# Kernel optimization log

Measured on AMD Instinct MI355X. Metric: run time of the kernel, lower is better.

Reference implementation:

```python
import jax, jax.numpy as jnp
import numpy as np

EPS = 1e-5  # RMSNorm epsilon


def rmsnorm(x, w):
    return x * jax.lax.rsqrt(jnp.mean(x * x, axis=-1, keepdims=True) + EPS) * w


def mamba_forward(u, in_proj_w, conv_w, conv_b, x_proj_w, dt_proj_w, dt_proj_b,
                  A_log, D_param, mamba_out_w):
    # u: (b, L, dm) -- canonical Mamba block (expand=2, d_state=16, d_conv=4)
    b, L, dm = u.shape
    di, ds = A_log.shape
    dtr = dt_proj_w.shape[1]
    xz = jnp.einsum('bld,ed->ble', u, in_proj_w)          # (b,L,2*di)
    x_, z = jnp.split(xz, 2, axis=-1)                     # each (b,L,di)
    # causal depthwise conv over the sequence axis
    dconv = conv_w.shape[-1]
    xc = jnp.transpose(x_, (0, 2, 1))                     # (b,di,L)
    xc = jnp.pad(xc, ((0, 0), (0, 0), (dconv - 1, 0)))
    xc = jax.lax.conv_general_dilated(xc, conv_w, window_strides=(1,), padding='VALID',
                                      dimension_numbers=('NCH', 'OIH', 'NCH'),
                                      feature_group_count=di)
    xc = xc + conv_b[None, :, None]
    x_ = jax.nn.silu(jnp.transpose(xc, (0, 2, 1)))        # (b,L,di)
    # input-dependent dt, B, C
    x_dbl = jnp.einsum('bld,ed->ble', x_, x_proj_w)       # (b,L,dtr+2*ds)
    dt, B, C = jnp.split(x_dbl, [dtr, dtr + ds], axis=-1)
    delta = jax.nn.softplus(jnp.einsum('blr,dr->bld', dt, dt_proj_w) + dt_proj_b)  # (b,L,di)
    A = -jnp.exp(A_log)                                   # (di,ds)

    def step(h, inp):
        d_t, B_t, C_t, x_t = inp                          # (b,di),(b,ds),(b,ds),(b,di)
        dA = jnp.exp(d_t[:, :, None] * A)                 # (b,di,ds)
        h = dA * h + (d_t * x_t)[:, :, None] * B_t[:, None, :]
        y = jnp.einsum('bds,bs->bd', h, C_t)
        return h, y

    xs = (jnp.moveaxis(delta, 1, 0), jnp.moveaxis(B, 1, 0),
          jnp.moveaxis(C, 1, 0), jnp.moveaxis(x_, 1, 0))
    h0 = jnp.zeros((b, di, ds), dtype=u.dtype)
    _, ys = jax.lax.scan(step, h0, xs)                    # ys: (L,b,di)
    y = jnp.moveaxis(ys, 0, 1) + x_ * D_param             # (b,L,di)
    y = y * jax.nn.silu(z)
    return jnp.einsum('bld,od->blo', y, mamba_out_w)      # (b,L,dm)


def conv1x1(W, bvec, t):
    # t: (b, cin, L) -> (b, cout, L)
    return jnp.einsum('oi,bit->bot', W, t) + bvec[None, :, None]


def reference(x, w_norm1, w_norm2, W_ip, b_ip, W_fp, b_fp, W_wp, b_wp, W_op, b_op,
              in_proj_w, conv_w, conv_b, x_proj_w, dt_proj_w, dt_proj_b,
              A_log, D_param, mamba_out_w):
    # x: (b, L, D) -- module's (b, c, l) with l == input_dim = D, c == seq = L
    residual = x
    xn = rmsnorm(x, w_norm1)                 # RMSNorm over last (input_dim) axis
    xt = jnp.transpose(xn, (0, 2, 1))        # 'b c l -> b l c' : (b, D, L)
    ssm = conv1x1(W_ip, b_ip, xt)            # (b, 2D, L)
    ssm = conv1x1(W_fp, b_fp, ssm)           # (b, 2D, L)
    u = jnp.transpose(ssm, (0, 2, 1))        # (b, L, 2D): seq=L, d_model=2D
    m = mamba_forward(u, in_proj_w, conv_w, conv_b, x_proj_w, dt_proj_w, dt_proj_b,
                      A_log, D_param, mamba_out_w)
    m = rmsnorm(m, w_norm2) + u              # PostNormMamba residual
    ssm = jnp.transpose(m, (0, 2, 1))        # (b, 2D, L)
    w = conv1x1(W_wp, b_wp, xt)              # (b, 2D, L)
    w = w * jax.nn.sigmoid(w)                # swish
    out = conv1x1(W_op, b_op, w * ssm)       # (b, D, L)
    return jnp.transpose(out, (0, 2, 1)) + residual


def setup_inputs():
    key = jax.random.key(0)
    ks = jax.random.split(key, 16)
    D, L, b = 64, 4096, 4
    dm, di, ds, dconv = 2 * D, 4 * D, 16, 4
    dtr = (dm + 15) // 16  # dt_rank = ceil(d_model/16) = 8

    def n(k, shape, fan_in):
        return jax.random.normal(k, shape, jnp.float32) * (1.0 / np.sqrt(fan_in))

    return {
        'x': jax.random.normal(ks[0], (b, L, D), jnp.float32),
        'w_norm1': jnp.ones((D,), jnp.float32),
        'w_norm2': jnp.ones((dm,), jnp.float32),
        'W_ip': n(ks[1], (2 * D, D), D), 'b_ip': jnp.zeros((2 * D,), jnp.float32),
        'W_fp': n(ks[2], (2 * D, 2 * D), 2 * D), 'b_fp': jnp.zeros((2 * D,), jnp.float32),
        'W_wp': n(ks[3], (2 * D, D), D), 'b_wp': jnp.zeros((2 * D,), jnp.float32),
        'W_op': n(ks[4], (D, 2 * D), 2 * D), 'b_op': jnp.zeros((D,), jnp.float32),
        'in_proj_w': n(ks[5], (2 * di, dm), dm),
        'conv_w': n(ks[6], (di, 1, dconv), dconv),
        'conv_b': jnp.zeros((di,), jnp.float32),
        'x_proj_w': n(ks[7], (dtr + 2 * ds, di), di),
        'dt_proj_w': n(ks[8], (di, dtr), dtr),
        'dt_proj_b': jnp.full((di,), float(np.log(np.expm1(0.01))), jnp.float32),
        'A_log': jnp.log(jnp.broadcast_to(jnp.arange(1, ds + 1, dtype=jnp.float32), (di, ds))),
        'D_param': jnp.ones((di,), jnp.float32),
        'mamba_out_w': n(ks[9], (dm, di), di),
    }
```

## Files before the change

### kernel.cpp

```cpp
#include <hip/hip_runtime.h>
#include <hip/hip_bf16.h>

typedef __hip_bfloat16 bf16;
typedef __attribute__((ext_vector_type(8))) short bf16x8;
typedef __attribute__((ext_vector_type(4))) float f32x4;
#define DEV __device__ __forceinline__

constexpr int SEQ  = 4096;
constexpr int NB   = 4;
constexpr int NTOK = NB * SEQ;
constexpr float EPS = 1e-5f;
constexpr int NCH = 32;
constexpr int NCHUNK = SEQ / NCH;
constexpr float LOG2E = 1.44269504f;

constexpr int OFF_WDT  = 0;
constexpr int OFF_WB   = 2048;
constexpr int WB_IP = 0;
constexpr int WB_WP = 8192;
constexpr int WB_FP = 16384;
constexpr int WB_PR = 32768;
constexpr int WB_MO = 98304;
constexpr int WB_OP = 131072;
constexpr int WB_XP = 139264;
constexpr int WB_TOT = 151552;
constexpr int OFF_XDBL = OFF_WB + WB_TOT / 2;
constexpr int OFF_R1   = OFF_XDBL + NTOK * 40;
constexpr int OFF_WSW  = OFF_R1   + 1048576;
constexpr int OFF_U    = OFF_WSW  + 1048576;
constexpr int OFF_R2   = OFF_U    + 1048576;
constexpr int OFF_SILUZ= OFF_R2   + 2097152;
constexpr int OFF_XC   = OFF_SILUZ+ 2097152;
constexpr int OFF_G    = OFF_XC   + 2097152;
constexpr int OFF_FLAG = OFF_G    + 2097152;
constexpr int OFF_SUMM = OFF_FLAG + 16;
constexpr int OFF_HIN  = OFF_SUMM + 64 * NCHUNK * 256 * 2;
constexpr int OFF_PLOC = OFF_HIN  + 64 * NCHUNK * 256;
constexpr int OFF_CUMD = OFF_PLOC + NTOK * 256;

DEV float b2f(bf16 x) { return __bfloat162float(x); }
DEV bf16 f2b(float x) { return __float2bfloat16(x); }
DEV short shof(bf16 h) { short s; __builtin_memcpy(&s, &h, 2); return s; }
DEV float ldin(const void* p, int i, int f) {
  return f ? ((const float*)p)[i] : b2f(((const bf16*)p)[i]);
}
DEV unsigned pack2(float a, float b) {
  bf16 ha = f2b(a), hb = f2b(b);
  unsigned short ua, ub;
  __builtin_memcpy(&ua, &ha, 2); __builtin_memcpy(&ub, &hb, 2);
  return (unsigned)ua | ((unsigned)ub << 16);
}
DEV float lo16f(unsigned u) { return __int_as_float((int)(u << 16)); }
DEV float hi16f(unsigned u) { return __int_as_float((int)(u & 0xffff0000u)); }
template<int CTRL>
DEV float dpp_add(float v) {
  int r = __builtin_amdgcn_update_dpp(0, __float_as_int(v), CTRL, 0xF, 0xF, false);
  return v + __int_as_float(r);
}
DEV float exp2f_fast(float a) { return __builtin_amdgcn_exp2f(a); }
DEV float softplus(float a) {
  return (a > 20.f) ? a : __logf(1.f + exp2f_fast(a * LOG2E));
}
DEV float silu(float a) { return a / (1.f + __expf(-a)); }

DEV void cpw(int e, int base, int count, const void* __restrict__ src,
             bf16* __restrict__ wb, int f) {
  int r = e - base;
  if (r >= 0 && r < count) wb[base + r] = f2b(ldin(src, r, f));
}
__global__ __launch_bounds__(256) void prep_k(
    const void* __restrict__ w_ip, const void* __restrict__ w_wp, const void* __restrict__ w_fp,
    const void* __restrict__ w_pr, const void* __restrict__ w_mo, const void* __restrict__ w_op,
    const void* __restrict__ w_x,  const void* __restrict__ w_dt,
    const void* __restrict__ x, float* __restrict__ wsf, int* __restrict__ flagp)
{
  __shared__ int cnt;
  if (threadIdx.x == 0) cnt = 0;
  __syncthreads();
  {
    float v = b2f(((const bf16*)x)[threadIdx.x]);
    int ok = (v == v) && fabsf(v) > 1e-4f && fabsf(v) < 100.f;
    atomicAdd(&cnt, ok);
  }
  __syncthreads();
  int f = (cnt > 204) ? 0 : 1;
  if (blockIdx.x == 0 && threadIdx.x == 0) *flagp = f;

  int e = blockIdx.x * 256 + threadIdx.x;
  bf16* wb = (bf16*)(wsf + OFF_WB);
  cpw(e, WB_IP, 8192,  w_ip, wb, f);
  cpw(e, WB_WP, 8192,  w_wp, wb, f);
  cpw(e, WB_FP, 16384, w_fp, wb, f);
  cpw(e, WB_PR, 65536, w_pr, wb, f);
  cpw(e, WB_MO, 32768, w_mo, wb, f);
  cpw(e, WB_OP, 8192,  w_op, wb, f);
  {
    int r = e - WB_XP;
    if (r >= 0 && r < 12288) wb[WB_XP + r] = (r < 10240) ? f2b(ldin(w_x, r, f)) : f2b(0.f);
  }
  if (e < 2048) {
    int r = e >> 8, d = e & 255;
    wsf[OFF_WDT + e] = ldin(w_dt, d * 8 + r, f);
  }
}

__global__ __launch_bounds__(512) void fm_k(
    const void* __restrict__ x, const void* __restrict__ w1, const float* __restrict__ wsf,
    const void* __restrict__ b_ip, const void* __restrict__ b_wp, const void* __restrict__ b_fp,
    bf16* __restrict__ wsw, bf16* __restrict__ u, bf16* __restrict__ xpre,
    bf16* __restrict__ siluz, const int* __restrict__ flagp)
{
  __shared__ __align__(16) char smem[33280];
  short* xn   = (short*)smem;
  short* t1   = (short*)(smem + 4608);
  short* ul   = (short*)(smem + 13312);
  short* wswl = (short*)(smem + 22016);
  short* xzl  = (short*)smem;

  const int f = *flagp;
  const int tid = threadIdx.x;
  const int tok0 = blockIdx.x * 32;
  {
    const int token = tid >> 4, r = tid & 15;
    float v[4]; float ss = 0.f;
    #pragma unroll
    for (int k = 0; k < 4; ++k) {
      v[k] = ldin(x, (tok0 + token) * 64 + r * 4 + k, f);
      ss += v[k] * v[k];
    }
    ss += __shfl_xor(ss, 1, 16); ss += __shfl_xor(ss, 2, 16);
    ss += __shfl_xor(ss, 4, 16); ss += __shfl_xor(ss, 8, 16);
    float sc = rsqrtf(ss * (1.f / 64.f) + EPS);
    unsigned* dst = (unsigned*)xn + token * 36 + r * 2;
    #pragma unroll
    for (int k = 0; k < 2; ++k) {
      int i = r * 4 + k * 2;
      dst[k] = pack2(v[k*2] * sc * ldin(w1, i, f), v[k*2+1] * sc * ldin(w1, i + 1, f));
    }
  }
  __syncthreads();
  const int lane = tid & 63, m = lane & 15, q = lane >> 4;
  const int w = tid >> 6;
  {
    const int wt = w >> 2, ng = w & 3;
    const bf16* W = (const bf16*)(wsf + OFF_WB) + (wt ? WB_WP : WB_IP);
    const void* bia = wt ? b_wp : b_ip;
    bf16x8 a[2][2];
    #pragma unroll
    for (int mt = 0; mt < 2; ++mt)
      #pragma unroll
      for (int kk = 0; kk < 2; ++kk)
        a[mt][kk] = *(const bf16x8*)&xn[(mt * 16 + m) * 72 + kk * 32 + q * 8];
    #pragma unroll
    for (int nti = 0; nti < 2; ++nti) {
      int nt = ng * 2 + nti;
      int n = nt * 16 + m;
      f32x4 acc[2] = {{0,0,0,0},{0,0,0,0}};
      #pragma unroll
      for (int kk = 0; kk < 2; ++kk) {
        bf16x8 b = *(const bf16x8*)(W + (nt * 16 + m) * 64 + kk * 32 + q * 8);
        #pragma unroll
        for (int mt = 0; mt < 2; ++mt)
          acc[mt] = __builtin_amdgcn_mfma_f32_16x16x32_bf16(a[mt][kk], b, acc[mt], 0, 0, 0);
      }
      float bv = ldin(bia, n, f);
      #pragma unroll
      for (int mt = 0; mt < 2; ++mt)
        #pragma unroll
        for (int r = 0; r < 4; ++r) {
          float v = acc[mt][r] + bv;
          int row = mt * 16 + q * 4 + r;
          if (wt) wswl[row * 128 + n] = shof(f2b(silu(v)));
          else    t1[row * 136 + n] = shof(f2b(v));
        }
    }
  }
  __syncthreads();
  {
    int row = tid >> 4, c8 = (tid & 15) * 8;
    uint4 v = *(const uint4*)&wswl[row * 128 + c8];
    *(uint4*)(wsw + (tok0 + row) * 128 + c8) = v;
  }
  {
    const bf16* WF = (const bf16*)(wsf + OFF_WB) + WB_FP;
    bf16x8 a[2][4];
    #pragma unroll
    for (int mt = 0; mt < 2; ++mt)
      #pragma unroll
      for (int kk = 0; kk < 4; ++kk)
        a[mt][kk] = *(const bf16x8*)&t1[(mt * 16 + m) * 136 + kk * 32 + q * 8];
    {
      int nt = w;
      int n = nt * 16 + m;
      f32x4 acc[2] = {{0,0,0,0},{0,0,0,0}};
      #pragma unroll
      for (int kk = 0; kk < 4; ++kk) {
        bf16x8 b = *(const bf16x8*)(WF + (nt * 16 + m) * 128 + kk * 32 + q * 8);
        #pragma unroll
        for (int mt = 0; mt < 2; ++mt)
          acc[mt] = __builtin_amdgcn_mfma_f32_16x16x32_bf16(a[mt][kk], b, acc[mt], 0, 0, 0);
      }
      float bv = ldin(b_fp, n, f);
      #pragma unroll
      for (int mt = 0; mt < 2; ++mt)
        #pragma unroll
        for (int r = 0; r < 4; ++r)
          ul[(mt * 16 + q * 4 + r) * 136 + n] = shof(f2b(acc[mt][r] + bv));
    }
  }
  __syncthreads();
  {
    int row = tid >> 4, c8 = (tid & 15) * 8;
    uint4 v = *(const uint4*)&ul[row * 136 + c8];
    *(uint4*)(u + (tok0 + row) * 128 + c8) = v;
  }
  {
    const bf16* WP = (const bf16*)(wsf + OFF_WB) + WB_PR;
    bf16x8 a[2][4];
    #pragma unroll
    for (int mt = 0; mt < 2; ++mt)
      #pragma unroll
      for (int kk = 0; kk < 4; ++kk)
        a[mt][kk] = *(const bf16x8*)&ul[(mt * 16 + m) * 136 + kk * 32 + q * 8];
    __syncthreads();
    #pragma unroll
    for (int nti = 0; nti < 4; ++nti) {
      int nt = w * 4 + nti;
      int n = nt * 16 + m;
      f32x4 acc[2] = {{0,0,0,0},{0,0,0,0}};
      #pragma unroll
      for (int kk = 0; kk < 4; ++kk) {
        bf16x8 b = *(const bf16x8*)(WP + (nt * 16 + m) * 128 + kk * 32 + q * 8);
        #pragma unroll
        for (int mt = 0; mt < 2; ++mt)
          acc[mt] = __builtin_amdgcn_mfma_f32_16x16x32_bf16(a[mt][kk], b, acc[mt], 0, 0, 0);
      }
      #pragma unroll
      for (int mt = 0; mt < 2; ++mt)
        #pragma unroll
        for (int r = 0; r < 4; ++r) {
          int row = mt * 16 + q * 4 + r;
          float v = acc[mt][r];
          xzl[row * 520 + n] = shof(f2b(n < 256 ? v : silu(v)));
        }
    }
  }
  __syncthreads();
  {
    #pragma unroll
    for (int k = 0; k < 4; ++k) {
      int chunk = tid + k * 512;
      int row = chunk >> 6, seg = chunk & 63;
      uint4 v = *(const uint4*)&xzl[row * 520 + seg * 8];
      int n0 = seg * 8;
      if (n0 < 256) *(uint4*)(xpre + (tok0 + row) * 256 + n0) = v;
      else          *(uint4*)(siluz + (tok0 + row) * 256 + (n0 - 256)) = v;
    }
  }
}

__global__ __launch_bounds__(256) void conv_k(
    const bf16* __restrict__ xpre, const void* __restrict__ cw, const void* __restrict__ cb,
    const float* __restrict__ wsf, bf16* __restrict__ xc, float* __restrict__ xdbl,
    const int* __restrict__ flagp)
{
  __shared__ short xh[35 * 256];
  __shared__ short cs[32 * 264];
  const int f = *flagp;
  const int tid = threadIdx.x;
  const int tok0 = blockIdx.x * 32;
  const bool seqstart = (tok0 & (SEQ - 1)) == 0;
  for (int c = tid; c < 1120; c += 256) {
    int e0 = c * 8;
    int tt = e0 >> 8, i = e0 & 255;
    int gtok = tok0 + tt - 3;
    uint4* dst = (uint4*)(xh + e0);
    if (gtok >= 0 && !(seqstart && tt < 3)) *dst = *(const uint4*)(xpre + gtok * 256 + i);
    else                                    *dst = make_uint4(0, 0, 0, 0);
  }
  __syncthreads();
  {
    const int ch0 = (tid & 63) * 4;
    const int t0 = (tid >> 6) * 8;
    float w4[4][4], cb4[4];
    #pragma unroll
    for (int c = 0; c < 4; ++c) {
      cb4[c] = ldin(cb, ch0 + c, f);
      #pragma unroll
      for (int k = 0; k < 4; ++k) w4[c][k] = ldin(cw, (ch0 + c) * 4 + k, f);
    }
    float win[11][4];
    #pragma unroll
    for (int r = 0; r < 11; ++r) {
      uint2 v = *(const uint2*)&xh[(t0 + r) * 256 + ch0];
      win[r][0] = lo16f(v.x); win[r][1] = hi16f(v.x);
      win[r][2] = lo16f(v.y); win[r][3] = hi16f(v.y);
    }
    #pragma unroll
    for (int t = 0; t < 8; ++t) {
      unsigned pk[2];
      #pragma unroll
      for (int cp = 0; cp < 2; ++cp) {
        float o[2];
        #pragma unroll
        for (int ci = 0; ci < 2; ++ci) {
          int c = cp * 2 + ci;
          float acc = cb4[c];
          #pragma unroll
          for (int k = 0; k < 4; ++k) acc = fmaf(win[t + k][c], w4[c][k], acc);
          o[ci] = silu(acc);
        }
        pk[cp] = pack2(o[0], o[1]);
      }
      uint2 pv = make_uint2(pk[0], pk[1]);
      *(uint2*)&cs[(t0 + t) * 264 + ch0] = pv;
      *(uint2*)(xc + (tok0 + t0 + t) * 256 + ch0) = pv;
    }
  }
  __syncthreads();
  const int w = tid >> 6;
  if (w < 2) {
    const bf16* Wx = (const bf16*)(wsf + OFF_WB) + WB_XP;
    const int lane = tid & 63, m = lane & 15, quad = lane >> 4;
    f32x4 acc[3] = {{0,0,0,0},{0,0,0,0},{0,0,0,0}};
    #pragma unroll
    for (int k0 = 0; k0 < 256; k0 += 32) {
      bf16x8 af = *(const bf16x8*)&cs[(w * 16 + m) * 264 + k0 + quad * 8];
      #pragma unroll
      for (int nt = 0; nt < 3; ++nt) {
        bf16x8 bfr = *(const bf16x8*)(Wx + (nt * 16 + m) * 256 + k0 + quad * 8);
        acc[nt] = __builtin_amdgcn_mfma_f32_16x16x32_bf16(af, bfr, acc[nt], 0, 0, 0);
      }
    }
    #pragma unroll
    for (int nt = 0; nt < 3; ++nt) {
      int n = nt * 16 + m;
      if (n < 40) {
        #pragma unroll
        for (int r = 0; r < 4; ++r)
          xdbl[(tok0 + w * 16 + quad * 4 + r) * 40 + n] = acc[nt][r];
      }
    }
  }
}

__global__ __launch_bounds__(256) void scanF_k(
    const float* __restrict__ xdbl, const bf16* __restrict__ xc,
    const void* __restrict__ A_log, const void* __restrict__ dt_b,
    const float* __restrict__ WDT, float* __restrict__ summ,
    float* __restrict__ ploc, float* __restrict__ cumd, const int* __restrict__ flagp)
{
  const int f = *flagp;
  const int tid = threadIdx.x;
  const int bb = blockIdx.x >> 2, dgsup = blockIdx.x & 3, c = blockIdx.y;
  const int dgsub = tid >> 6, lane = tid & 63, dl = lane >> 2, squad = lane & 3;
  const int dg = dgsup * 4 + dgsub;
  const int bxOld = bb * 16 + dg;
  const int d_comp = dg * 16 + dl;
  const int bd = tid & 63;
  const int d_stg = dgsup * 64 + bd;
  const int bdc = dgsub * 16 + dl;
  const int tok_base = bb * SEQ + c * NCH;

  __shared__ float dt_l[NCH * 8];
  __shared__ float dx_l[16 * 64 * 2];
  __shared__ float Bp[16 * 16];
  __shared__ float Cp[16 * 16];
  __shared__ float pg_l[16 * 64];
  __shared__ float cd_l[16 * 64];

  float Aval2[4];
  #pragma unroll
  for (int j = 0; j < 4; ++j)
    Aval2[j] = -__expf(ldin(A_log, d_comp * 16 + squad * 4 + j, f)) * LOG2E;
  const float dtb_stg = ldin(dt_b, d_stg, f);
  float wdt[8];
  #pragma unroll
  for (int r = 0; r < 8; ++r) wdt[r] = WDT[r * 256 + d_stg];

  float h[4] = {0.f, 0.f, 0.f, 0.f};
  float sdlt = 0.f;

  if (tid < 64)
    *(float4*)(dt_l + tid * 4) = *(const float4*)(xdbl + (tok_base + (tid >> 1)) * 40 + (tid & 1) * 4);

  #pragma unroll 1
  for (int half = 0; half < 2; ++half) {
    const int tb = half * 16;
    __syncthreads();
    {
      int tl = tid >> 4, s = tid & 15;
      int tok = tok_base + tb + tl;
      Bp[tid] = xdbl[tok * 40 + 8 + s];
      Cp[tid] = xdbl[tok * 40 + 24 + s];
    }
    #pragma unroll
    for (int k = 0; k < 4; ++k) {
      int tl = (tid >> 6) + k * 4;
      int tok = tok_base + tb + tl;
      const float* dtr = dt_l + (tb + tl) * 8;
      float a = dtb_stg;
      #pragma unroll
      for (int r = 0; r < 8; ++r) a = fmaf(dtr[r], wdt[r], a);
      float dlt = softplus(a);
      float xcv = b2f(xc[tok * 256 + d_stg]);
      *(float2*)(dx_l + (tl * 64 + bd) * 2) = make_float2(dlt, dlt * xcv);
    }
    __syncthreads();

    #pragma unroll 8
    for (int tl = 0; tl < 16; ++tl) {
      float2 dx = *(const float2*)(dx_l + (tl * 64 + bdc) * 2);
      float4 B4 = *(const float4*)(Bp + tl * 16 + squad * 4);
      float Bv[4] = {B4.x, B4.y, B4.z, B4.w};
      #pragma unroll
      for (int j = 0; j < 4; ++j) {
        float dA = exp2f_fast(dx.x * Aval2[j]);
        h[j] = fmaf(dA, h[j], dx.y * Bv[j]);
      }
      sdlt += dx.x;
      float4 C4 = *(const float4*)(Cp + tl * 16 + squad * 4);
      float p = h[0] * C4.x;
      p = fmaf(h[1], C4.y, p);
      p = fmaf(h[2], C4.z, p);
      p = fmaf(h[3], C4.w, p);
      p = dpp_add<0xB1>(p);
      p = dpp_add<0x4E>(p);
      if (squad == 0) { pg_l[tl * 64 + bdc] = p; cd_l[tl * 64 + bdc] = sdlt; }
    }
    __syncthreads();
    #pragma unroll
    for (int k = 0; k < 4; ++k) {
      int tl = (tid >> 6) + k * 4;
      int tok = tok_base + tb + tl;
      ploc[tok * 256 + d_stg] = pg_l[tl * 64 + bd];
      cumd[tok * 256 + d_stg] = cd_l[tl * 64 + bd];
    }
  }

  float* dst = summ + ((bxOld * NCHUNK + c) * 256 + dl * 16 + squad * 4) * 2;
  *(float4*)(dst)     = make_float4(exp2f_fast(Aval2[0] * sdlt), h[0],
                                    exp2f_fast(Aval2[1] * sdlt), h[1]);
  *(float4*)(dst + 4) = make_float4(exp2f_fast(Aval2[2] * sdlt), h[2],
                                    exp2f_fast(Aval2[3] * sdlt), h[3]);
}

__global__ __launch_bounds__(256) void scanB_k(const float* __restrict__ summ, float* __restrict__ hinit) {
  int bx = blockIdx.x, qq = threadIdx.x;
  float h = 0.f;
  for (int c0 = 0; c0 < NCHUNK; c0 += 16) {
    float2 sv[16];
    #pragma unroll
    for (int k = 0; k < 16; ++k)
      sv[k] = *(const float2*)(summ + ((bx * NCHUNK + c0 + k) * 256 + qq) * 2);
    #pragma unroll
    for (int k = 0; k < 16; ++k) {
      hinit[(bx * NCHUNK + c0 + k) * 256 + qq] = h;
      h = fmaf(sv[k].x, h, sv[k].y);
    }
  }
}

__global__ __launch_bounds__(256) void scanC_k(
    const float* __restrict__ xdbl, const bf16* __restrict__ xc, const bf16* __restrict__ siluz,
    const void* __restrict__ A_log, const void* __restrict__ D_par,
    const float* __restrict__ hinit, const float* __restrict__ ploc,
    const float* __restrict__ cumd, bf16* __restrict__ g, const int* __restrict__ flagp)
{
  const int f = *flagp;
  const int tid = threadIdx.x;
  const int bb = blockIdx.x >> 2, dgsup = blockIdx.x & 3, c = blockIdx.y;
  const int dgsub = tid >> 6, lane = tid & 63, dl = lane >> 2, squad = lane & 3;
  const int dg = dgsup * 4 + dgsub;
  const int bxOld = bb * 16 + dg;
  const int d_comp = dg * 16 + dl;
  const int bd = tid & 63;
  const int d_stg = dgsup * 64 + bd;
  const int bdc = dgsub * 16 + dl;
  const int tok_base = bb * SEQ + c * NCH;

  __shared__ float Cp[NCH * 16];
  __shared__ float cd_l[NCH * 64];
  __shared__ float g_l[NCH * 64];

  float Aval2[4];
  #pragma unroll
  for (int j = 0; j < 4; ++j)
    Aval2[j] = -__expf(ldin(A_log, d_comp * 16 + squad * 4 + j, f)) * LOG2E;
  const float Dp_stg = ldin(D_par, d_stg, f);

  float4 hv = *(const float4*)(hinit + (bxOld * NCHUNK + c) * 256 + dl * 16 + squad * 4);

  #pragma unroll
  for (int k = 0; k < 2; ++k) {
    int e = tid + k * 256;
    int tl = e >> 4, s = e & 15;
    Cp[e] = xdbl[(tok_base + tl) * 40 + 24 + s];
  }
  #pragma unroll
  for (int k = 0; k < 8; ++k) {
    int tl = (tid >> 6) + k * 4;
    cd_l[tl * 64 + bd] = cumd[(tok_base + tl) * 256 + d_stg];
  }
  __syncthreads();

  #pragma unroll 8
  for (int tl = 0; tl < NCH; ++tl) {
    float cum = cd_l[tl * 64 + bdc];
    float4 C4 = *(const float4*)(Cp + tl * 16 + squad * 4);
    float p =      C4.x * exp2f_fast(cum * Aval2[0]) * hv.x;
    p = fmaf(C4.y * exp2f_fast(cum * Aval2[1]), hv.y, p);
    p = fmaf(C4.z * exp2f_fast(cum * Aval2[2]), hv.z, p);
    p = fmaf(C4.w * exp2f_fast(cum * Aval2[3]), hv.w, p);
    p = dpp_add<0xB1>(p);
    p = dpp_add<0x4E>(p);
    if (squad == 0) g_l[tl * 64 + bdc] = p;
  }
  __syncthreads();

  #pragma unroll
  for (int k = 0; k < 8; ++k) {
    int tl = (tid >> 6) + k * 4;
    int tok = tok_base + tl;
    float pf = ploc[tok * 256 + d_stg] + g_l[tl * 64 + bd];
    float xcv = b2f(xc[tok * 256 + d_stg]);
    g[tok * 256 + d_stg] = f2b((pf + xcv * Dp_stg) * b2f(siluz[tok * 256 + d_stg]));
  }
}

__global__ __launch_bounds__(512) void back_k(
    const bf16* __restrict__ g, const float* __restrict__ wsf, const void* __restrict__ w2,
    const bf16* __restrict__ u, const bf16* __restrict__ wsw, const void* __restrict__ b_op,
    const void* __restrict__ x, void* __restrict__ out, const int* __restrict__ flagp)
{
  __shared__ __align__(16) short ms[32 * 136];
  const int f = *flagp;
  const int tid = threadIdx.x;
  const int tok0 = blockIdx.x * 32;
  const int lane = tid & 63, m = lane & 15, q = lane >> 4;
  const int w = tid >> 6;
  const bf16* WM = (const bf16*)(wsf + OFF_WB) + WB_MO;
  const bf16* WO = (const bf16*)(wsf + OFF_WB) + WB_OP;
  {
    f32x4 acc[2] = {{0,0,0,0},{0,0,0,0}};
    #pragma unroll
    for (int kk = 0; kk < 8; ++kk) {
      bf16x8 a0 = *(const bf16x8*)(g + (tok0 + m) * 256 + kk * 32 + q * 8);
      bf16x8 a1 = *(const bf16x8*)(g + (tok0 + 16 + m) * 256 + kk * 32 + q * 8);
      int nt = w;
      bf16x8 b = *(const bf16x8*)(WM + (nt * 16 + m) * 256 + kk * 32 + q * 8);
      acc[0] = __builtin_amdgcn_mfma_f32_16x16x32_bf16(a0, b, acc[0], 0, 0, 0);
      acc[1] = __builtin_amdgcn_mfma_f32_16x16x32_bf16(a1, b, acc[1], 0, 0, 0);
    }
    {
      int n = w * 16 + m;
      #pragma unroll
      for (int mt = 0; mt < 2; ++mt)
        #pragma unroll
        for (int r = 0; r < 4; ++r)
          ms[(mt * 16 + q * 4 + r) * 136 + n] = shof(f2b(acc[mt][r]));
    }
  }
  __syncthreads();
  {
    const int token = tid >> 4, r = tid & 15;
    float mv[8]; float ss = 0.f;
    #pragma unroll
    for (int k = 0; k < 8; ++k) {
      mv[k] = b2f(((const bf16*)ms)[token * 136 + r * 8 + k]);
      ss += mv[k] * mv[k];
    }
    ss += __shfl_xor(ss, 1, 16); ss += __shfl_xor(ss, 2, 16);
    ss += __shfl_xor(ss, 4, 16); ss += __shfl_xor(ss, 8, 16);
    float sc = rsqrtf(ss * (1.f / 128.f) + EPS);
    #pragma unroll
    for (int k = 0; k < 8; ++k) {
      int i = r * 8 + k;
      int ga = (tok0 + token) * 128 + i;
      float v = mv[k] * sc * ldin(w2, i, f) + b2f(u[ga]);
      ms[token * 136 + i] = shof(f2b(v * b2f(wsw[ga])));
    }
  }
  __syncthreads();
  {
    const int mt = w >> 2, nt = w & 3;
    bf16x8 a[4];
    #pragma unroll
    for (int kk = 0; kk < 4; ++kk)
      a[kk] = *(const bf16x8*)&ms[(mt * 16 + m) * 136 + kk * 32 + q * 8];
    __syncthreads();
    f32x4 acc = {0,0,0,0};
    #pragma unroll
    for (int kk = 0; kk < 4; ++kk) {
      bf16x8 b = *(const bf16x8*)(WO + (nt * 16 + m) * 128 + kk * 32 + q * 8);
      acc = __builtin_amdgcn_mfma_f32_16x16x32_bf16(a[kk], b, acc, 0, 0, 0);
    }
    float* outl = (float*)ms;
    int n = nt * 16 + m;
    #pragma unroll
    for (int r = 0; r < 4; ++r)
      outl[(mt * 16 + q * 4 + r) * 68 + n] = acc[r];
  }
  __syncthreads();
  {
    const float* outl = (const float*)ms;
    int row = tid >> 4, c0 = (tid & 15) * 4;
    float v[4];
    #pragma unroll
    for (int j = 0; j < 4; ++j)
      v[j] = outl[row * 68 + c0 + j] + ldin(b_op, c0 + j, f)
           + ldin(x, (tok0 + row) * 64 + c0 + j, f);
    if (f) {
      *(float4*)((float*)out + (tok0 + row) * 64 + c0) = make_float4(v[0], v[1], v[2], v[3]);
    } else {
      uint2 pv = make_uint2(pack2(v[0], v[1]), pack2(v[2], v[3]));
      *(uint2*)((bf16*)out + (tok0 + row) * 64 + c0) = pv;
    }
  }
}

extern "C" void kernel_launch(void* const* d_in, const int* in_sizes, int n_in,
                              void* d_out, int out_size, void* d_ws, size_t ws_size,
                              hipStream_t stream) {
  (void)in_sizes; (void)n_in; (void)out_size; (void)ws_size;
  const void* x        = d_in[0];
  const void* w_norm1  = d_in[1];
  const void* w_norm2  = d_in[2];
  const void* W_ip     = d_in[3];
  const void* b_ip     = d_in[4];
  const void* W_fp     = d_in[5];
  const void* b_fp     = d_in[6];
  const void* W_wp     = d_in[7];
  const void* b_wp     = d_in[8];
  const void* W_op     = d_in[9];
  const void* b_op     = d_in[10];
  const void* in_proj  = d_in[11];
  const void* conv_w   = d_in[12];
  const void* conv_b   = d_in[13];
  const void* x_proj   = d_in[14];
  const void* dt_projw = d_in[15];
  const void* dt_projb = d_in[16];
  const void* A_log    = d_in[17];
  const void* D_par    = d_in[18];
  const void* mo_w     = d_in[19];

  float* wsf    = (float*)d_ws;
  float* xdbl   = wsf + OFF_XDBL;
  bf16*  wsw_b  = (bf16*)(wsf + OFF_WSW);
  bf16*  u_b    = (bf16*)(wsf + OFF_U);
  bf16*  xpre_b = (bf16*)(wsf + OFF_R2);
  float* summ   = wsf + OFF_SUMM;
  float* hin    = wsf + OFF_HIN;
  float* plocp  = wsf + OFF_PLOC;
  float* cumdp  = wsf + OFF_CUMD;
  bf16*  siluz_b= (bf16*)(wsf + OFF_SILUZ);
  bf16*  xc_b   = (bf16*)(wsf + OFF_XC);
  bf16*  g_b    = (bf16*)(wsf + OFF_G);
  int*   flagp  = (int*)(wsf + OFF_FLAG);

  prep_k<<<dim3(592), dim3(256), 0, stream>>>(W_ip, W_wp, W_fp, in_proj, mo_w, W_op,
                                              x_proj, dt_projw, x, wsf, flagp);
  fm_k<<<dim3(NTOK / 32), dim3(512), 0, stream>>>(x, w_norm1, wsf, b_ip, b_wp, b_fp,
                                                  wsw_b, u_b, xpre_b, siluz_b, flagp);
  conv_k<<<dim3(NTOK / 32), dim3(256), 0, stream>>>(xpre_b, conv_w, conv_b, wsf, xc_b, xdbl, flagp);
  scanF_k<<<dim3(16, NCHUNK), dim3(256), 0, stream>>>(xdbl, xc_b, A_log, dt_projb,
                                                      wsf + OFF_WDT, summ, plocp, cumdp, flagp);
  scanB_k<<<dim3(64), dim3(256), 0, stream>>>(summ, hin);
  scanC_k<<<dim3(16, NCHUNK), dim3(256), 0, stream>>>(xdbl, xc_b, siluz_b, A_log, D_par,
                                                      hin, plocp, cumdp, g_b, flagp);
  back_k<<<dim3(NTOK / 32), dim3(512), 0, stream>>>(g_b, wsf, w_norm2, u_b, wsw_b, b_op, x, d_out, flagp);
}
```

Baseline: 198.4 us.

## Fuse scan combine stage into output projection kernel, keeping g in LDS

Merges the scanC kernel, which applies the chunk initial state, adds D*x and gates with silu(z), into the back kernel. Each 32-token block now computes the gated output for all 256 channels in two passes and holds it in shared memory for the MFMA out-projection. This removes the global write and re-read of the g tensor and one kernel launch. The cost is much more LDS per block (about 51KB), which may lower occupancy, plus extra barriers and serial per-channel-half passes inside each block.

```diff
diff --git a/kernel.cpp b/kernel.cpp
--- a/kernel.cpp
+++ b/kernel.cpp
@@ -461,92 +461,88 @@
   }
 }
 
-__global__ __launch_bounds__(256) void scanC_k(
+__global__ __launch_bounds__(512) void backC_k(
     const float* __restrict__ xdbl, const bf16* __restrict__ xc, const bf16* __restrict__ siluz,
     const void* __restrict__ A_log, const void* __restrict__ D_par,
-    const float* __restrict__ hinit, const float* __restrict__ ploc,
-    const float* __restrict__ cumd, bf16* __restrict__ g, const int* __restrict__ flagp)
-{
-  const int f = *flagp;
-  const int tid = threadIdx.x;
-  const int bb = blockIdx.x >> 2, dgsup = blockIdx.x & 3, c = blockIdx.y;
-  const int dgsub = tid >> 6, lane = tid & 63, dl = lane >> 2, squad = lane & 3;
-  const int dg = dgsup * 4 + dgsub;
-  const int bxOld = bb * 16 + dg;
-  const int d_comp = dg * 16 + dl;
-  const int bd = tid & 63;
-  const int d_stg = dgsup * 64 + bd;
-  const int bdc = dgsub * 16 + dl;
-  const int tok_base = bb * SEQ + c * NCH;
-
-  __shared__ float Cp[NCH * 16];
-  __shared__ float cd_l[NCH * 64];
-  __shared__ float g_l[NCH * 64];
-
-  float Aval2[4];
-  #pragma unroll
-  for (int j = 0; j < 4; ++j)
-    Aval2[j] = -__expf(ldin(A_log, d_comp * 16 + squad * 4 + j, f)) * LOG2E;
-  const float Dp_stg = ldin(D_par, d_stg, f);
-
-  float4 hv = *(const float4*)(hinit + (bxOld * NCHUNK + c) * 256 + dl * 16 + squad * 4);
-
-  #pragma unroll
-  for (int k = 0; k < 2; ++k) {
-    int e = tid + k * 256;
-    int tl = e >> 4, s = e & 15;
-    Cp[e] = xdbl[(tok_base + tl) * 40 + 24 + s];
-  }
-  #pragma unroll
-  for (int k = 0; k < 8; ++k) {
-    int tl = (tid >> 6) + k * 4;
-    cd_l[tl * 64 + bd] = cumd[(tok_base + tl) * 256 + d_stg];
-  }
-  __syncthreads();
-
-  #pragma unroll 8
-  for (int tl = 0; tl < NCH; ++tl) {
-    float cum = cd_l[tl * 64 + bdc];
-    float4 C4 = *(const float4*)(Cp + tl * 16 + squad * 4);
-    float p =      C4.x * exp2f_fast(cum * Aval2[0]) * hv.x;
-    p = fmaf(C4.y * exp2f_fast(cum * Aval2[1]), hv.y, p);
-    p = fmaf(C4.z * exp2f_fast(cum * Aval2[2]), hv.z, p);
-    p = fmaf(C4.w * exp2f_fast(cum * Aval2[3]), hv.w, p);
-    p = dpp_add<0xB1>(p);
-    p = dpp_add<0x4E>(p);
-    if (squad == 0) g_l[tl * 64 + bdc] = p;
-  }
-  __syncthreads();
-
-  #pragma unroll
-  for (int k = 0; k < 8; ++k) {
-    int tl = (tid >> 6) + k * 4;
-    int tok = tok_base + tl;
-    float pf = ploc[tok * 256 + d_stg] + g_l[tl * 64 + bd];
-    float xcv = b2f(xc[tok * 256 + d_stg]);
-    g[tok * 256 + d_stg] = f2b((pf + xcv * Dp_stg) * b2f(siluz[tok * 256 + d_stg]));
-  }
-}
-
-__global__ __launch_bounds__(512) void back_k(
-    const bf16* __restrict__ g, const float* __restrict__ wsf, const void* __restrict__ w2,
+    const float* __restrict__ hinit, const float* __restrict__ ploc, const float* __restrict__ cumd,
+    const float* __restrict__ wsf, const void* __restrict__ w2,
     const bf16* __restrict__ u, const bf16* __restrict__ wsw, const void* __restrict__ b_op,
     const void* __restrict__ x, void* __restrict__ out, const int* __restrict__ flagp)
 {
-  __shared__ __align__(16) short ms[32 * 136];
+  __shared__ __align__(16) char smem[51712];
+  short* gl  = (short*)smem;
+  float* Cp  = (float*)(smem + 16896);
+  float* cdl = (float*)(smem + 18944);
+  float* gcl = (float*)(smem + 35328);
+  short* ms  = (short*)(smem + 18944);
+
   const int f = *flagp;
   const int tid = threadIdx.x;
   const int tok0 = blockIdx.x * 32;
-  const int lane = tid & 63, m = lane & 15, q = lane >> 4;
-  const int w = tid >> 6;
+  const int bb = tok0 >> 12;
+  const int c  = (tok0 & (SEQ - 1)) >> 5;
+  const int w = tid >> 6, lane = tid & 63;
+  const int dl = lane >> 2, squad = lane & 3;
+  const int chL = w * 16 + dl;
+  const int chE = tid & 127;
+
+  {
+    int tl = tid >> 4, s = tid & 15;
+    Cp[tid] = xdbl[(tok0 + tl) * 40 + 24 + s];
+  }
+
+  #pragma unroll 1
+  for (int p = 0; p < 2; ++p) {
+    const int ch = p * 128 + chL;
+    #pragma unroll
+    for (int k = 0; k < 8; ++k) {
+      int tl = (tid >> 7) + k * 4;
+      cdl[tl * 128 + chE] = cumd[(tok0 + tl) * 256 + p * 128 + chE];
+    }
+    float Aval2[4];
+    #pragma unroll
+    for (int j = 0; j < 4; ++j)
+      Aval2[j] = -__expf(ldin(A_log, ch * 16 + squad * 4 + j, f)) * LOG2E;
+    float4 hv = *(const float4*)(hinit +
+        ((bb * 16 + (ch >> 4)) * NCHUNK + c) * 256 + (ch & 15) * 16 + squad * 4);
+    __syncthreads();
+    #pragma unroll 8
+    for (int tl = 0; tl < 32; ++tl) {
+      float cum = cdl[tl * 128 + chL];
+      float4 C4 = *(const float4*)(Cp + tl * 16 + squad * 4);
+      float pv =      C4.x * exp2f_fast(cum * Aval2[0]) * hv.x;
+      pv = fmaf(C4.y * exp2f_fast(cum * Aval2[1]), hv.y, pv);
+      pv = fmaf(C4.z * exp2f_fast(cum * Aval2[2]), hv.z, pv);
+      pv = fmaf(C4.w * exp2f_fast(cum * Aval2[3]), hv.w, pv);
+      pv = dpp_add<0xB1>(pv);
+      pv = dpp_add<0x4E>(pv);
+      if (squad == 0) gcl[tl * 128 + chL] = pv;
+    }
+    __syncthreads();
+    {
+      const int gch = p * 128 + chE;
+      const float Dp = ldin(D_par, gch, f);
+      #pragma unroll
+      for (int k = 0; k < 8; ++k) {
+        int tl = (tid >> 7) + k * 4;
+        int tok = tok0 + tl;
+        float pf = gcl[tl * 128 + chE] + ploc[tok * 256 + gch];
+        float xcv = b2f(xc[tok * 256 + gch]);
+        gl[tl * 264 + gch] = shof(f2b((pf + xcv * Dp) * b2f(siluz[tok * 256 + gch])));
+      }
+    }
+    __syncthreads();
+  }
+
+  const int m = lane & 15, q = lane >> 4;
   const bf16* WM = (const bf16*)(wsf + OFF_WB) + WB_MO;
   const bf16* WO = (const bf16*)(wsf + OFF_WB) + WB_OP;
   {
     f32x4 acc[2] = {{0,0,0,0},{0,0,0,0}};
     #pragma unroll
     for (int kk = 0; kk < 8; ++kk) {
-      bf16x8 a0 = *(const bf16x8*)(g + (tok0 + m) * 256 + kk * 32 + q * 8);
-      bf16x8 a1 = *(const bf16x8*)(g + (tok0 + 16 + m) * 256 + kk * 32 + q * 8);
+      bf16x8 a0 = *(const bf16x8*)&gl[m * 264 + kk * 32 + q * 8];
+      bf16x8 a1 = *(const bf16x8*)&gl[(16 + m) * 264 + kk * 32 + q * 8];
       int nt = w;
       bf16x8 b = *(const bf16x8*)(WM + (nt * 16 + m) * 256 + kk * 32 + q * 8);
       acc[0] = __builtin_amdgcn_mfma_f32_16x16x32_bf16(a0, b, acc[0], 0, 0, 0);
@@ -655,7 +651,6 @@
   float* cumdp  = wsf + OFF_CUMD;
   bf16*  siluz_b= (bf16*)(wsf + OFF_SILUZ);
   bf16*  xc_b   = (bf16*)(wsf + OFF_XC);
-  bf16*  g_b    = (bf16*)(wsf + OFF_G);
   int*   flagp  = (int*)(wsf + OFF_FLAG);
 
   prep_k<<<dim3(592), dim3(256), 0, stream>>>(W_ip, W_wp, W_fp, in_proj, mo_w, W_op,
@@ -666,7 +661,7 @@
   scanF_k<<<dim3(16, NCHUNK), dim3(256), 0, stream>>>(xdbl, xc_b, A_log, dt_projb,
                                                       wsf + OFF_WDT, summ, plocp, cumdp, flagp);
   scanB_k<<<dim3(64), dim3(256), 0, stream>>>(summ, hin);
-  scanC_k<<<dim3(16, NCHUNK), dim3(256), 0, stream>>>(xdbl, xc_b, siluz_b, A_log, D_par,
-                                                      hin, plocp, cumdp, g_b, flagp);
-  back_k<<<dim3(NTOK / 32), dim3(512), 0, stream>>>(g_b, wsf, w_norm2, u_b, wsw_b, b_op, x, d_out, flagp);
-}
+  backC_k<<<dim3(NTOK / 32), dim3(512), 0, stream>>>(xdbl, xc_b, siluz_b, A_log, D_par,
+                                                     hin, plocp, cumdp, wsf, w_norm2,
+                                                     u_b, wsw_b, b_op, x, d_out, flagp);
+}
```

Result: faster. 188.4 us (-5.0%).
